# Performance work log

Measured on AMD Instinct MI355X. Metric: run time of the kernel, lower is better.

Reference implementation:

```python
import jax, jax.numpy as jnp
import numpy as np
import math

D_MODEL = 64
D_STATE = 16
V_RANGE = 1
K = 3
BATCH, H, W = 4, 32, 32
V_LIST = [(x, y) for x in range(-V_RANGE, V_RANGE + 1) for y in range(-V_RANGE, V_RANGE + 1)]
NUM_V = len(V_LIST)


def _circ_conv(x, w):
    # x: (B, Cin, H, W), w: (Cout, Cin, K, K); circular padding then VALID conv
    p = K // 2
    xp = jnp.pad(x, ((0, 0), (0, 0), (p, p), (p, p)), mode='wrap')
    return jax.lax.conv_general_dilated(
        xp, w, window_strides=(1, 1), padding='VALID',
        dimension_numbers=('NCHW', 'OIHW', 'NCHW'))


def setup_inputs() -> dict:
    key = jax.random.key(0)
    ks = jax.random.split(key, 8)
    fan = 1.0 / math.sqrt(D_MODEL * K * K)
    u_t = jax.random.normal(ks[0], (BATCH, D_MODEL, H, W), dtype=jnp.float32)
    s_prev = jax.random.normal(ks[1], (BATCH, NUM_V, D_MODEL, D_STATE, H, W), dtype=jnp.float32)
    conv_delta_w = jax.random.normal(ks[2], (D_MODEL, D_MODEL, K, K), dtype=jnp.float32) * fan
    conv_delta_b = jax.random.normal(ks[3], (D_MODEL,), dtype=jnp.float32) * 0.01
    conv_B_w = jax.random.normal(ks[4], (D_STATE, D_MODEL, K, K), dtype=jnp.float32) * fan
    conv_C_w = jax.random.normal(ks[5], (D_STATE, D_MODEL, K, K), dtype=jnp.float32) * fan
    log_A_real = jnp.log(0.5 * jnp.ones((D_MODEL, D_STATE), dtype=jnp.float32))
    D = jnp.ones((D_MODEL,), dtype=jnp.float32)
    dt_inv_softplus = jnp.asarray(math.log(math.e - 1.0), dtype=jnp.float32)
    return {
        'u_t': u_t, 's_prev': s_prev,
        'conv_delta_w': conv_delta_w, 'conv_delta_b': conv_delta_b,
        'conv_B_w': conv_B_w, 'conv_C_w': conv_C_w,
        'log_A_real': log_A_real, 'D': D, 'dt_inv_softplus': dt_inv_softplus,
    }


def reference(u_t, s_prev, conv_delta_w, conv_delta_b, conv_B_w, conv_C_w,
              log_A_real, D, dt_inv_softplus):
    # delta: (B, d_model, h, w)
    delta = jax.nn.softplus(_circ_conv(u_t, conv_delta_w)
                            + conv_delta_b[None, :, None, None] + dt_inv_softplus)
    B_val = _circ_conv(u_t, conv_B_w)   # (B, d_state, h, w)
    C_val = _circ_conv(u_t, conv_C_w)   # (B, d_state, h, w)
    A = -jnp.exp(log_A_real)            # (d_model, d_state)
    A_bc = A[None, :, :, None, None]    # (1, d_model, d_state, 1, 1)
    A_bar = jnp.exp(delta[:, :, None] * A_bc)        # (B, d_model, d_state, h, w)
    B_bar = (A_bar - 1.0) / A_bc * B_val[:, None]    # (B, d_model, d_state, h, w)
    u_bc = u_t[:, :, None]              # (B, d_model, 1, h, w)
    C_bc = C_val[:, None]               # (B, 1, d_state, h, w)
    y_skip = u_t * D[None, :, None, None]

    s_next_list, y_list = [], []
    for i, (vx, vy) in enumerate(V_LIST):
        s_tr = jnp.roll(s_prev[:, i], shift=(-vy, -vx), axis=(-2, -1))
        s_new = A_bar * s_tr + B_bar * u_bc          # (B, d_model, d_state, h, w)
        y_new = jnp.sum(s_new * C_bc, axis=2) + y_skip
        s_next_list.append(s_new)
        y_list.append(y_new)
    s_next = jnp.stack(s_next_list, axis=1)  # (B, num_v, d_model, d_state, h, w)
    y_out = jnp.stack(y_list, axis=1)        # (B, num_v, d_model, h, w)
    return (y_out, s_next)
```

## Files before the change

kernel.cpp:

```cpp
#include <hip/hip_runtime.h>
#include <math.h>

#define NBATCH 4
#define NV 9
#define DM 64
#define DS 16

__device__ __forceinline__ float softplus_f(float x) {
    return (x > 20.f) ? x : log1pf(__expf(x));
}

__device__ __forceinline__ void nt_store_f2(float* p, float x, float y) {
    unsigned long long v = (unsigned long long)__float_as_uint(x)
                         | ((unsigned long long)__float_as_uint(y) << 32);
    __builtin_nontemporal_store(v, (unsigned long long*)p);
}

__global__ __launch_bounds__(256) void conv_kernel(
    const float* __restrict__ u, const float* __restrict__ wd,
    const float* __restrict__ bd, const float* __restrict__ wb,
    const float* __restrict__ wc, const float* __restrict__ dtp,
    float* __restrict__ delta_out, float* __restrict__ Bv_out,
    float* __restrict__ Cv_out)
{
    int bx = blockIdx.x;
    int ht = bx & 3;
    int co = (bx >> 2) % 96;
    int b  = bx / 384;
    int tid = threadIdx.x;
    int chunk = __builtin_amdgcn_readfirstlane(tid >> 6);
    int pxt = tid & 63;
    int row = ht * 8 + (pxt >> 3);
    int w0  = (pxt & 7) << 2;

    const float* wbase = (co < 64) ? (wd + (size_t)co * 576)
                       : (co < 80) ? (wb + (size_t)(co - 64) * 576)
                                   : (wc + (size_t)(co - 80) * 576);

    int hm = (row + 31) & 31, hp = (row + 1) & 31;
    int wl = (w0 + 31) & 31;
    int wr = (w0 + 4) & 31;
    const float* ub = u + (size_t)b * 65536 + (size_t)(chunk << 4) * 1024;
    const float* wq0 = wbase + (size_t)(chunk << 4) * 9;

    float a0 = 0.f, a1 = 0.f, a2 = 0.f, a3 = 0.f;
    #pragma unroll 4
    for (int j = 0; j < 16; ++j) {
        const float* base = ub + j * 1024;
        const float* wq = wq0 + j * 9;
        #pragma unroll
        for (int r = 0; r < 3; ++r) {
            int rr = (r == 0) ? hm : (r == 1) ? row : hp;
            const float* rp = base + rr * 32;
            float4 v = *(const float4*)(rp + w0);
            float L = rp[wl], R = rp[wr];
            float k0 = wq[r * 3 + 0], k1 = wq[r * 3 + 1], k2 = wq[r * 3 + 2];
            a0 = fmaf(k0, L,   fmaf(k1, v.x, fmaf(k2, v.y, a0)));
            a1 = fmaf(k0, v.x, fmaf(k1, v.y, fmaf(k2, v.z, a1)));
            a2 = fmaf(k0, v.y, fmaf(k1, v.z, fmaf(k2, v.w, a2)));
            a3 = fmaf(k0, v.z, fmaf(k1, v.w, fmaf(k2, R,   a3)));
        }
    }

    __shared__ float4 part[4][64];
    part[chunk][pxt] = make_float4(a0, a1, a2, a3);
    __syncthreads();

    if (tid < 64) {
        float4 p0 = part[0][tid], p1 = part[1][tid];
        float4 p2 = part[2][tid], p3 = part[3][tid];
        float s0 = p0.x + p1.x + p2.x + p3.x;
        float s1 = p0.y + p1.y + p2.y + p3.y;
        float s2 = p0.z + p1.z + p2.z + p3.z;
        float s3 = p0.w + p1.w + p2.w + p3.w;
        int prow = ht * 8 + (tid >> 3);
        int pw   = (tid & 7) << 2;
        int pix  = prow * 32 + pw;
        if (co < 64) {
            float bias = bd[co] + dtp[0];
            float4 o;
            o.x = softplus_f(s0 + bias);
            o.y = softplus_f(s1 + bias);
            o.z = softplus_f(s2 + bias);
            o.w = softplus_f(s3 + bias);
            *(float4*)(delta_out + (((size_t)b * 64 + co) << 10) + pix) = o;
        } else if (co < 80) {
            *(float4*)(Bv_out + (((size_t)b * 16 + (co - 64)) << 10) + pix) =
                make_float4(s0, s1, s2, s3);
        } else {
            *(float4*)(Cv_out + (((size_t)b * 16 + (co - 80)) << 10) + pix) =
                make_float4(s0, s1, s2, s3);
        }
    }
}

__global__ __launch_bounds__(256) void scan_kernel(
    const float* __restrict__ u, const float* __restrict__ s_prev,
    const float* __restrict__ logA, const float* __restrict__ Dp,
    const float* __restrict__ delta_in, const float* __restrict__ Bv,
    const float* __restrict__ Cv,
    float* __restrict__ y_out, float* __restrict__ s_next)
{
    int bx = blockIdx.x;
    int half = bx & 1;
    int c  = (bx >> 1) & 63;
    int bi9 = bx >> 7;
    int i  = bi9 % 9;
    int b  = bi9 / 9;

    int tid = threadIdx.x;
    int pix0 = ((half << 8) + tid) << 1;
    int h  = pix0 >> 5;
    int w0 = pix0 & 31;
    int vx = i / 3 - 1;
    int vy = i % 3 - 1;
    int hh = (h + vy + 32) & 31;

    int lane = tid & 63;
    int lnext = (lane & ~15) | ((lane + 1) & 15);
    int lprev = (lane & ~15) | ((lane + 15) & 15);

    __shared__ float sA[16], srA[16];
    if (tid < 16) {
        float A = -__expf(logA[c * 16 + tid]);
        sA[tid]  = A;
        srA[tid] = __builtin_amdgcn_rcpf(A);
    }
    __syncthreads();

    size_t ubase = (((size_t)b * 64 + c) << 10) + pix0;
    float2 u2 = *(const float2*)(u + ubase);
    float2 d2 = *(const float2*)(delta_in + ubase);
    float dk = Dp[c];
    float yx = u2.x * dk, yy = u2.y * dk;

    size_t chan = ((size_t)bi9 * 64 + c) * 16;
    const float* sp_row = s_prev + (chan << 10) + hh * 32 + w0;
    float*       sn_px  = s_next + (chan << 10) + pix0;
    const float* bvp = Bv + (((size_t)b * 16) << 10) + pix0;
    const float* cvp = Cv + (((size_t)b * 16) << 10) + pix0;

    #pragma unroll 4
    for (int n = 0; n < 16; ++n) {
        float A  = sA[n];
        float rA = srA[n];

        float2 b2 = *(const float2*)(bvp + ((size_t)n << 10));
        float2 c2 = *(const float2*)(cvp + ((size_t)n << 10));
        float2 f  = *(const float2*)(sp_row + ((size_t)n << 10));

        float abx = __expf(d2.x * A);
        float aby = __expf(d2.y * A);
        float bux = (abx - 1.f) * rA * b2.x * u2.x;
        float buy = (aby - 1.f) * rA * b2.y * u2.y;

        float sx, sy;
        if (vx == 0) {
            sx = f.x; sy = f.y;
        } else if (vx > 0) {
            sx = f.y; sy = __shfl(f.x, lnext);
        } else {
            sx = __shfl(f.y, lprev); sy = f.x;
        }

        float snx = fmaf(abx, sx, bux);
        float sny = fmaf(aby, sy, buy);
        nt_store_f2(sn_px + ((size_t)n << 10), snx, sny);

        yx = fmaf(snx, c2.x, yx);
        yy = fmaf(sny, c2.y, yy);
    }
    nt_store_f2(y_out + (((size_t)bi9 * 64 + c) << 10) + pix0, yx, yy);
}

extern "C" void kernel_launch(void* const* d_in, const int* in_sizes, int n_in,
                              void* d_out, int out_size, void* d_ws, size_t ws_size,
                              hipStream_t stream) {
    const float* u      = (const float*)d_in[0];
    const float* s_prev = (const float*)d_in[1];
    const float* wd     = (const float*)d_in[2];
    const float* bd     = (const float*)d_in[3];
    const float* wb     = (const float*)d_in[4];
    const float* wc     = (const float*)d_in[5];
    const float* logA   = (const float*)d_in[6];
    const float* Dp     = (const float*)d_in[7];
    const float* dtp    = (const float*)d_in[8];

    float* ws    = (float*)d_ws;
    float* delta = ws;
    float* Bv    = ws + 262144;
    float* Cv    = ws + 327680;

    float* y_out  = (float*)d_out;
    float* s_next = y_out + (size_t)NBATCH * NV * DM * 1024;

    conv_kernel<<<dim3(4 * 96 * 4), dim3(256), 0, stream>>>(
        u, wd, bd, wb, wc, dtp, delta, Bv, Cv);
    scan_kernel<<<dim3(4 * 9 * 64 * 2), dim3(256), 0, stream>>>(
        u, s_prev, logA, Dp, delta, Bv, Cv, y_out, s_next);
}
```

Measured before the change: 102.0 us.

## Use one pixel per thread in scan and precompute A table in prep kernel

```diff
diff --git a/kernel.cpp b/kernel.cpp
--- a/kernel.cpp
+++ b/kernel.cpp
@@ -10,10 +10,10 @@
     return (x > 20.f) ? x : log1pf(__expf(x));
 }
 
-__device__ __forceinline__ void nt_store_f2(float* p, float x, float y) {
-    unsigned long long v = (unsigned long long)__float_as_uint(x)
-                         | ((unsigned long long)__float_as_uint(y) << 32);
-    __builtin_nontemporal_store(v, (unsigned long long*)p);
+__global__ void prep_kernel(const float* __restrict__ logA, float2* __restrict__ Atab) {
+    int t = threadIdx.x;
+    float A = -__expf(logA[t]);
+    Atab[t] = make_float2(A, __builtin_amdgcn_rcpf(A));
 }
 
 __global__ __launch_bounds__(256) void conv_kernel(
@@ -96,81 +96,52 @@
 
 __global__ __launch_bounds__(256) void scan_kernel(
     const float* __restrict__ u, const float* __restrict__ s_prev,
-    const float* __restrict__ logA, const float* __restrict__ Dp,
+    const float2* __restrict__ Atab, const float* __restrict__ Dp,
     const float* __restrict__ delta_in, const float* __restrict__ Bv,
     const float* __restrict__ Cv,
     float* __restrict__ y_out, float* __restrict__ s_next)
 {
     int bx = blockIdx.x;
-    int half = bx & 1;
-    int c  = (bx >> 1) & 63;
-    int bi9 = bx >> 7;
+    int t  = bx & 3;
+    int c  = (bx >> 2) & 63;
+    int bi9 = bx >> 8;
     int i  = bi9 % 9;
     int b  = bi9 / 9;
 
     int tid = threadIdx.x;
-    int pix0 = ((half << 8) + tid) << 1;
-    int h  = pix0 >> 5;
-    int w0 = pix0 & 31;
+    int pix = (t << 8) + tid;
+    int h = pix >> 5, w = pix & 31;
+
     int vx = i / 3 - 1;
     int vy = i % 3 - 1;
     int hh = (h + vy + 32) & 31;
+    int ww = (w + vx + 32) & 31;
 
-    int lane = tid & 63;
-    int lnext = (lane & ~15) | ((lane + 1) & 15);
-    int lprev = (lane & ~15) | ((lane + 15) & 15);
+    size_t ub = (((size_t)b * 64 + c) << 10) + pix;
+    float uv = u[ub];
+    float dv = delta_in[ub];
+    float y  = uv * Dp[c];
 
-    __shared__ float sA[16], srA[16];
-    if (tid < 16) {
-        float A = -__expf(logA[c * 16 + tid]);
-        sA[tid]  = A;
-        srA[tid] = __builtin_amdgcn_rcpf(A);
+    size_t chan = (((size_t)bi9 * 64 + c) << 4);
+    const float* sp  = s_prev + (chan << 10) + hh * 32 + ww;
+    float*       sn  = s_next + (chan << 10) + pix;
+    const float* bvp = Bv + (((size_t)b << 14)) + pix;
+    const float* cvp = Cv + (((size_t)b << 14)) + pix;
+    const float2* at = Atab + (c << 4);
+
+    #pragma unroll
+    for (int n = 0; n < 16; ++n) {
+        float2 Ar = at[n];
+        float s  = sp[n << 10];
+        float bval = bvp[n << 10];
+        float cval = cvp[n << 10];
+        float ab = __expf(dv * Ar.x);
+        float bu = (ab - 1.f) * Ar.y * bval * uv;
+        float v  = fmaf(ab, s, bu);
+        __builtin_nontemporal_store(v, sn + (n << 10));
+        y = fmaf(v, cval, y);
     }
-    __syncthreads();
-
-    size_t ubase = (((size_t)b * 64 + c) << 10) + pix0;
-    float2 u2 = *(const float2*)(u + ubase);
-    float2 d2 = *(const float2*)(delta_in + ubase);
-    float dk = Dp[c];
-    float yx = u2.x * dk, yy = u2.y * dk;
-
-    size_t chan = ((size_t)bi9 * 64 + c) * 16;
-    const float* sp_row = s_prev + (chan << 10) + hh * 32 + w0;
-    float*       sn_px  = s_next + (chan << 10) + pix0;
-    const float* bvp = Bv + (((size_t)b * 16) << 10) + pix0;
-    const float* cvp = Cv + (((size_t)b * 16) << 10) + pix0;
-
-    #pragma unroll 4
-    for (int n = 0; n < 16; ++n) {
-        float A  = sA[n];
-        float rA = srA[n];
-
-        float2 b2 = *(const float2*)(bvp + ((size_t)n << 10));
-        float2 c2 = *(const float2*)(cvp + ((size_t)n << 10));
-        float2 f  = *(const float2*)(sp_row + ((size_t)n << 10));
-
-        float abx = __expf(d2.x * A);
-        float aby = __expf(d2.y * A);
-        float bux = (abx - 1.f) * rA * b2.x * u2.x;
-        float buy = (aby - 1.f) * rA * b2.y * u2.y;
-
-        float sx, sy;
-        if (vx == 0) {
-            sx = f.x; sy = f.y;
-        } else if (vx > 0) {
-            sx = f.y; sy = __shfl(f.x, lnext);
-        } else {
-            sx = __shfl(f.y, lprev); sy = f.x;
-        }
-
-        float snx = fmaf(abx, sx, bux);
-        float sny = fmaf(aby, sy, buy);
-        nt_store_f2(sn_px + ((size_t)n << 10), snx, sny);
-
-        yx = fmaf(snx, c2.x, yx);
-        yy = fmaf(sny, c2.y, yy);
-    }
-    nt_store_f2(y_out + (((size_t)bi9 * 64 + c) << 10) + pix0, yx, yy);
+    __builtin_nontemporal_store(y, y_out + (((size_t)bi9 * 64 + c) << 10) + pix);
 }
 
 extern "C" void kernel_launch(void* const* d_in, const int* in_sizes, int n_in,
@@ -190,12 +161,14 @@
     float* delta = ws;
     float* Bv    = ws + 262144;
     float* Cv    = ws + 327680;
+    float2* Atab = (float2*)(ws + 393216);
 
     float* y_out  = (float*)d_out;
     float* s_next = y_out + (size_t)NBATCH * NV * DM * 1024;
 
+    prep_kernel<<<dim3(1), dim3(1024), 0, stream>>>(logA, Atab);
     conv_kernel<<<dim3(4 * 96 * 4), dim3(256), 0, stream>>>(
         u, wd, bd, wb, wc, dtp, delta, Bv, Cv);
-    scan_kernel<<<dim3(4 * 9 * 64 * 2), dim3(256), 0, stream>>>(
-        u, s_prev, logA, Dp, delta, Bv, Cv, y_out, s_next);
+    scan_kernel<<<dim3(4 * 9 * 64 * 4), dim3(256), 0, stream>>>(
+        u, s_prev, Atab, Dp, delta, Bv, Cv, y_out, s_next);
 }
```

After: 105.9 us. 3.8% more time.
